# Kernel optimization log

Measured on AMD Instinct MI355X. Metric: run time of the kernel, lower is better.

The kernel has to match this reference:

```python
import jax, jax.numpy as jnp
import numpy as np

K = 20
EPS = 1e-5


def graph_feature(x, k=K):
    # x: [B, C, N] -> [B, 2C, N, k] (DGCNN edge features)
    xt = jnp.transpose(x, (0, 2, 1))                      # [B, N, C]
    sq = jnp.sum(xt * xt, axis=-1)                        # [B, N]
    inner = jnp.einsum('bnc,bmc->bnm', xt, xt)            # [B, N, N]
    neg_dist = 2.0 * inner - sq[:, :, None] - sq[:, None, :]
    idx = jax.lax.top_k(neg_dist, k)[1]                   # [B, N, k]
    nbr = jax.vmap(lambda f, i: f[i])(xt, idx)            # [B, N, k, C]
    ctr = jnp.broadcast_to(xt[:, :, None, :], nbr.shape)
    feat = jnp.concatenate([nbr - ctr, ctr], axis=-1)     # [B, N, k, 2C]
    return jnp.transpose(feat, (0, 3, 1, 2))              # [B, 2C, N, k]


def conv_bn_relu(x, W, g, b):
    # 1x1 conv (channel matmul) + BatchNorm (batch stats, training mode) + ReLU
    y = jnp.einsum('oc,bcnk->bonk', W, x)
    m = jnp.mean(y, axis=(0, 2, 3), keepdims=True)
    v = jnp.var(y, axis=(0, 2, 3), keepdims=True)
    yn = (y - m) * jax.lax.rsqrt(v + EPS)
    return jax.nn.relu(yn * g[None, :, None, None] + b[None, :, None, None])


def setup_inputs() -> dict:
    key = jax.random.key(0)
    ks = jax.random.split(key, 12)
    d = {'x': jax.random.normal(ks[0], (8, 3, 2048), dtype=jnp.float32)}
    chans = [(6, 64), (64, 64), (64, 128), (128, 256), (512, 512)]
    for i, (cin, cout) in enumerate(chans):
        d[f'W{i+1}'] = jax.random.normal(ks[i + 1], (cout, cin), dtype=jnp.float32) * (1.0 / np.sqrt(cin))
        d[f'g{i+1}'] = jnp.ones((cout,), dtype=jnp.float32)
        d[f'b{i+1}'] = jnp.zeros((cout,), dtype=jnp.float32)
    return d


def reference(x, W1, g1, b1, W2, g2, b2, W3, g3, b3, W4, g4, b4, W5, g5, b5):
    B, C, N = x.shape
    h = graph_feature(x)                                  # [B, 6, N, k]
    h = conv_bn_relu(h, W1, g1, b1)
    x1 = jnp.max(h, axis=-1, keepdims=True)               # [B, 64, N, 1]
    h = conv_bn_relu(h, W2, g2, b2)
    x2 = jnp.max(h, axis=-1, keepdims=True)
    h = conv_bn_relu(h, W3, g3, b3)
    x3 = jnp.max(h, axis=-1, keepdims=True)
    h = conv_bn_relu(h, W4, g4, b4)
    x4 = jnp.max(h, axis=-1, keepdims=True)
    cat = jnp.concatenate([x1, x2, x3, x4], axis=1)       # [B, 512, N, 1]
    out = conv_bn_relu(cat, W5, g5, b5)                   # [B, 512, N, 1]
    return out.reshape(B, -1, N)
```

## Files before the change

### kernel.cpp

```cpp
#include <hip/hip_runtime.h>
#include <hip/hip_bf16.h>

typedef _Float16 f16;
typedef _Float16 f16x8 __attribute__((ext_vector_type(8)));
typedef _Float16 f16x4 __attribute__((ext_vector_type(4)));
typedef float    f32x4 __attribute__((ext_vector_type(4)));
typedef unsigned long long u64;

constexpr int NB  = 8;
constexpr int NPT = 2048;
constexpr int KK  = 20;
constexpr int PT  = NB * NPT * KK;
constexpr int BNP = NB * NPT;
constexpr float EPS_BN = 1e-5f;
constexpr int NREP = 64;

constexpr size_t OFF_IDX = 0;
constexpr size_t OFF_WT1 = OFF_IDX + (size_t)BNP * KK * 4;
constexpr size_t OFF_WH2 = OFF_WT1 + 384 * 4;
constexpr size_t OFF_WH3 = OFF_WH2 + 4096 * 2;
constexpr size_t OFF_WH4 = OFF_WH3 + 8192 * 2;
constexpr size_t OFF_WH5 = OFF_WH4 + 32768 * 2;
constexpr size_t OFF_ST  = OFF_WH5 + 262144 * 2;
constexpr size_t OFF_SS  = OFF_ST + 5 * 1024 * 4;
constexpr size_t OFF_CAT = OFF_SS + 5 * 1024 * 4;
constexpr size_t OFF_Y3  = OFF_CAT + (size_t)BNP * 512 * 2;
constexpr size_t OFF_Y1  = OFF_Y3 + (size_t)PT * 64 * 2;
constexpr size_t OFF_Y2  = OFF_Y3 + (size_t)PT * 128 * 2;
constexpr size_t OFF_REP = OFF_Y2 + (size_t)PT * 64 * 2;
constexpr size_t WS_NEED = OFF_REP + (size_t)NREP * 1024 * 4;

__global__ void marker_kernel(float* __restrict__ out, float v) {
    if (threadIdx.x == 0 && blockIdx.x == 0) out[0] = v;
}

__device__ __forceinline__ void gload16(const f16* g, f16* ldsbase) {
    __builtin_amdgcn_global_load_lds(
        (const __attribute__((address_space(1))) void*)g,
        (__attribute__((address_space(3))) void*)ldsbase, 16, 0, 0);
}

__global__ __launch_bounds__(256) void prep_weights(
        const float* __restrict__ W1, const float* __restrict__ W2,
        const float* __restrict__ W3, const float* __restrict__ W4,
        const float* __restrict__ W5,
        float* __restrict__ wt1, f16* __restrict__ wh2, f16* __restrict__ wh3,
        f16* __restrict__ wh4, f16* __restrict__ wh5) {
    int i = blockIdx.x * 256 + threadIdx.x;
    if (i < 384)    { int o = i / 6, c = i - o * 6; wt1[c * 64 + o] = W1[i]; }
    if (i < 4096)   wh2[i] = (f16)W2[i];
    if (i < 8192)   wh3[i] = (f16)W3[i];
    if (i < 32768)  wh4[i] = (f16)W4[i];
    if (i < 262144) wh5[i] = (f16)W5[i];
}

__device__ __forceinline__ u64 mkkey(float d, int m) {
    unsigned u = __float_as_uint(d);
    u = (u & 0x80000000u) ? ~u : (u | 0x80000000u);
    return ((u64)u << 32) | (unsigned)(2047 - m);
}
__device__ __forceinline__ int key2m(u64 k) { return 2047 - (int)(k & 0xFFFFFFFFull); }

__device__ __forceinline__ void qins(u64 k, u64& q0, u64& q1, u64& q2, u64& q3, u64& spill) {
    bool c0 = k > q0, c1 = k > q1, c2 = k > q2, c3 = k > q3;
    u64 drop = c3 ? q3 : k;
    spill = spill > drop ? spill : drop;
    q3 = c2 ? q2 : (c3 ? k : q3);
    q2 = c1 ? q1 : (c2 ? k : q2);
    q1 = c0 ? q0 : (c1 ? k : q1);
    q0 = c0 ? k  : q0;
}

__global__ __launch_bounds__(256) void knn_kernel(const float* __restrict__ x,
                                                  int* __restrict__ idxo) {
    const int tid  = threadIdx.x;
    const int lane = tid & 63;
    const int wid  = tid >> 6;
    const int r    = blockIdx.x * 4 + wid;
    const int b    = r >> 11;
    const int n    = r & 2047;
    const float* xb = x + b * (3 * NPT);

    __shared__ float sqs[NPT];
    __shared__ int   cand[4][32];
#pragma unroll
    for (int i = 0; i < NPT / 256; ++i) {
        int m = i * 256 + tid;
        float a0 = xb[m], a1 = xb[NPT + m], a2 = xb[2 * NPT + m];
        sqs[m] = __fadd_rn(__fadd_rn(__fmul_rn(a0, a0), __fmul_rn(a1, a1)),
                           __fmul_rn(a2, a2));
    }
    __syncthreads();

    const float xn0 = xb[n], xn1 = xb[NPT + n], xn2 = xb[2 * NPT + n];
    const float sqn = sqs[n];

    auto dist2 = [&](int m) -> float {
        float dot = __fmaf_rn(xn0, xb[m],
                    __fmaf_rn(xn1, xb[NPT + m],
                    __fmul_rn(xn2, xb[2 * NPT + m])));
        return __fsub_rn(__fsub_rn(__fmul_rn(2.f, dot), sqn), sqs[m]);
    };

    u64 qa0 = 0, qa1 = 0, qa2 = 0, qa3 = 0, sA = 0;
    u64 qb0 = 0, qb1 = 0, qb2 = 0, qb3 = 0, sB = 0;
#pragma unroll
    for (int i = 0; i < 16; ++i) {
        int ma = i * 64 + lane;
        int mb = 1024 + ma;
        float da = dist2(ma);
        float db = dist2(mb);
        qins(mkkey(da, ma), qa0, qa1, qa2, qa3, sA);
        qins(mkkey(db, mb), qb0, qb1, qb2, qb3, sB);
    }
    u64 spill = sA > sB ? sA : sB;
    qins(qb0, qa0, qa1, qa2, qa3, spill);
    qins(qb1, qa0, qa1, qa2, qa3, spill);
    qins(qb2, qa0, qa1, qa2, qa3, spill);
    qins(qb3, qa0, qa1, qa2, qa3, spill);
    u64 q0 = qa0, q1 = qa1, q2 = qa2, q3 = qa3;

    int C;
    unsigned lo = 0u, hi = 0xFFFFFFFFu;
#pragma unroll 1
    for (int it = 0; it < 32 && lo < hi; ++it) {
        unsigned span = hi - lo;
        unsigned mid  = lo + (span >> 1) + (span & 1);
        u64 M = (u64)mid << 32;
        int cnt = __popcll(__ballot(q0 >= M)) + __popcll(__ballot(q1 >= M))
                + __popcll(__ballot(q2 >= M)) + __popcll(__ballot(q3 >= M));
        if (cnt >= 26) lo = mid; else hi = mid - 1;
    }
    const u64 T64 = (u64)lo << 32;

    u64 b0 = __ballot(q0 >= T64), b1 = __ballot(q1 >= T64);
    u64 b2 = __ballot(q2 >= T64), b3 = __ballot(q3 >= T64);
    int n0 = __popcll(b0), n1 = __popcll(b1), n2 = __popcll(b2), n3 = __popcll(b3);
    C = n0 + n1 + n2 + n3;
    bool conflict = (__ballot(spill >= T64) != 0ull) || (C > 32);

    if (!conflict) {
        u64 ltm = (1ull << lane) - 1ull;
        if (q0 >= T64) cand[wid][__popcll(b0 & ltm)] = key2m(q0);
        if (q1 >= T64) cand[wid][n0 + __popcll(b1 & ltm)] = key2m(q1);
        if (q2 >= T64) cand[wid][n0 + n1 + __popcll(b2 & ltm)] = key2m(q2);
        if (q3 >= T64) cand[wid][n0 + n1 + n2 + __popcll(b3 & ltm)] = key2m(q3);
    } else {
        C = 26;
#pragma unroll 1
        for (int t = 0; t < 26; ++t) {
            u64 v = q0;
#pragma unroll
            for (int s = 1; s < 64; s <<= 1) {
                u64 ov = __shfl_xor(v, s);
                if (ov > v) v = ov;
            }
            if (lane == 0) cand[wid][t] = key2m(v);
            if (q0 == v) {
                q0 = q1; q1 = q2; q2 = q3; q3 = 0;
                if (!(q0 > spill)) {
                    q0 = q1 = q2 = q3 = 0; spill = 0;
                    for (int ii = 0; ii < 32; ++ii) {
                        int mr = ii * 64 + lane;
                        u64 kr = mkkey(dist2(mr), mr);
                        if (kr < v) qins(kr, q0, q1, q2, q3, spill);
                    }
                }
            }
        }
    }
    __syncthreads();

    int mm = (lane < C) ? cand[wid][lane] : 0;
    const double dxn0 = (double)xn0, dxn1 = (double)xn1, dxn2 = (double)xn2;
    const double dsqn = dxn0 * dxn0 + dxn1 * dxn1 + dxn2 * dxn2;
    double xm0 = (double)xb[mm], xm1 = (double)xb[NPT + mm], xm2 = (double)xb[2 * NPT + mm];
    double ddot = dxn0 * xm0 + dxn1 * xm1 + dxn2 * xm2;
    double dsqm = xm0 * xm0 + xm1 * xm1 + xm2 * xm2;
    double dd   = 2.0 * ddot - dsqn - dsqm;

    int rank = 0;
#pragma unroll 1
    for (int s = 0; s < C; ++s) {
        double ds = __shfl(dd, s);
        int    ms = __shfl(mm, s);
        if (ds > dd || (ds == dd && ms < mm)) ++rank;
    }
    if (lane < C && rank < KK) idxo[rank * BNP + r] = mm;
}

__global__ __launch_bounds__(256) void conv1_kernel(const float* __restrict__ x,
                                                    const int* __restrict__ idx,
                                                    const float* __restrict__ Wt,
                                                    f16* __restrict__ y,
                                                    float* __restrict__ strep) {
    const int tid = threadIdx.x, lane = tid & 63, wid = tid >> 6;
    int p = blockIdx.x * 256 + tid;
    int r = p & (BNP - 1);
    int n = r & 2047;
    int b = r >> 11;
    int m = idx[p];
    const float* xb = x + b * (3 * NPT);
    float f3 = xb[n], f4 = xb[NPT + n], f5 = xb[2 * NPT + n];
    float f0 = xb[m] - f3, f1 = xb[NPT + m] - f4, f2 = xb[2 * NPT + m] - f5;
    float fv[6] = { f0, f1, f2, f3, f4, f5 };

    float acc[64];
#pragma unroll
    for (int o = 0; o < 64; ++o) acc[o] = 0.f;
#pragma unroll
    for (int c = 0; c < 6; ++c) {
        float hv = fv[c];
#pragma unroll
        for (int o = 0; o < 64; ++o) acc[o] = fmaf(Wt[c * 64 + o], hv, acc[o]);
    }
    f16* yp = y + (size_t)p * 64;
#pragma unroll
    for (int o = 0; o < 64; ++o) yp[o] = (f16)acc[o];

    __shared__ float lsum[4][64], lsq[4][64];
#pragma unroll
    for (int o = 0; o < 64; ++o) {
        float s = acc[o], q = acc[o] * acc[o];
#pragma unroll
        for (int off = 32; off >= 1; off >>= 1) { s += __shfl_xor(s, off); q += __shfl_xor(q, off); }
        if (lane == 0) { lsum[wid][o] = s; lsq[wid][o] = q; }
    }
    __syncthreads();
    float* rep = strep + ((blockIdx.x & (NREP - 1)) << 10);
    if (tid < 64) {
        atomicAdd(rep + tid,       lsum[0][tid] + lsum[1][tid] + lsum[2][tid] + lsum[3][tid]);
        atomicAdd(rep + 512 + tid, lsq[0][tid] + lsq[1][tid] + lsq[2][tid] + lsq[3][tid]);
    }
}

template<int CIN, int OBW>
__global__ __launch_bounds__(256) void conv_mfma_kernel(const f16* __restrict__ h,
                                                        const f16* __restrict__ W,
                                                        const f16* __restrict__ scshH,
                                                        f16* __restrict__ y,
                                                        float* __restrict__ strep) {
    constexpr int COUT = OBW * 64;
    const int tid = threadIdx.x, lane = tid & 63, wid = tid >> 6;
    const int lr = lane & 15, lg = lane >> 4;
    const int p0 = blockIdx.x * (256 / OBW) + (wid / OBW) * 64;
    const int ob = (wid & (OBW - 1)) * 64;

    f16x8 Bn[CIN / 32][4];
#pragma unroll
    for (int kt = 0; kt < CIN / 32; ++kt) {
        const int koff = kt * 32 + lg * 8;
        f16x8 scf = *(const f16x8*)(scshH + koff);
        f16x8 shf = *(const f16x8*)(scshH + 512 + koff);
#pragma unroll
        for (int pt = 0; pt < 4; ++pt) {
            f16x8 raw = *(const f16x8*)(h + (size_t)(p0 + pt * 16 + lr) * CIN + koff);
            f16x8 t = raw * scf + shf;
            f16x8 Bv;
#pragma unroll
            for (int e = 0; e < 8; ++e)
                Bv[e] = t[e] > (f16)0.f ? t[e] : (f16)0.f;
            Bn[kt][pt] = Bv;
        }
    }

    f32x4 acc[4][4];
#pragma unroll
    for (int pt = 0; pt < 4; ++pt)
#pragma unroll
        for (int t = 0; t < 4; ++t) acc[pt][t] = (f32x4){0.f, 0.f, 0.f, 0.f};

#pragma unroll
    for (int kt = 0; kt < CIN / 32; ++kt) {
        const int koff = kt * 32 + lg * 8;
        f16x8 A[4];
#pragma unroll
        for (int t = 0; t < 4; ++t)
            A[t] = *(const f16x8*)(W + (size_t)(ob + 16 * t + lr) * CIN + koff);
#pragma unroll
        for (int pt = 0; pt < 4; ++pt)
#pragma unroll
            for (int t = 0; t < 4; ++t)
                acc[pt][t] = __builtin_amdgcn_mfma_f32_16x16x32_f16(A[t], Bn[kt][pt], acc[pt][t], 0, 0, 0);
    }
#pragma unroll
    for (int pt = 0; pt < 4; ++pt) {
        int px = p0 + pt * 16 + lr;
#pragma unroll
        for (int t = 0; t < 4; ++t) {
            f16x4 v;
            v[0] = (f16)acc[pt][t][0]; v[1] = (f16)acc[pt][t][1];
            v[2] = (f16)acc[pt][t][2]; v[3] = (f16)acc[pt][t][3];
            *(f16x4*)(y + (size_t)px * COUT + ob + 16 * t + 4 * lg) = v;
        }
    }
    __shared__ float lsum[4][64], lsq[4][64];
#pragma unroll
    for (int t = 0; t < 4; ++t)
#pragma unroll
        for (int j = 0; j < 4; ++j) {
            float s = acc[0][t][j] + acc[1][t][j] + acc[2][t][j] + acc[3][t][j];
            float q = acc[0][t][j] * acc[0][t][j] + acc[1][t][j] * acc[1][t][j]
                    + acc[2][t][j] * acc[2][t][j] + acc[3][t][j] * acc[3][t][j];
#pragma unroll
            for (int m2 = 1; m2 < 16; m2 <<= 1) { s += __shfl_xor(s, m2); q += __shfl_xor(q, m2); }
            if (lr == 0) { lsum[wid][16 * t + 4 * lg + j] = s; lsq[wid][16 * t + 4 * lg + j] = q; }
        }
    __syncthreads();
    float* rep = strep + ((blockIdx.x & (NREP - 1)) << 10);
    if (tid < COUT) {
        int obIdx = tid >> 6, c = tid & 63;
        float S = 0.f, Q = 0.f;
#pragma unroll
        for (int w = obIdx; w < 4; w += OBW) { S += lsum[w][c]; Q += lsq[w][c]; }
        atomicAdd(rep + tid, S);
        atomicAdd(rep + 512 + tid, Q);
    }
}

__global__ __launch_bounds__(256) void conv4_fused_mfma(const f16* __restrict__ h,
                                                        const f16* __restrict__ W,
                                                        const f16* __restrict__ scshH,
                                                        float* __restrict__ strep,
                                                        f16* __restrict__ mx4,
                                                        f16* __restrict__ mn4,
                                                        f16* __restrict__ cat) {
    const int tid = threadIdx.x, lane = tid & 63, wid = tid >> 6;
    const int lr = lane & 15, lg = lane >> 4;
    const int r0 = blockIdx.x * 16;
    const int ob = wid * 64;

    __shared__ f16 sb[2][4][16][128];

    f32x4 rmax[4], rmin[4], rsum[4], rsq[4];
#pragma unroll
    for (int t = 0; t < 4; ++t) {
        rmax[t] = (f32x4){-3.3e38f, -3.3e38f, -3.3e38f, -3.3e38f};
        rmin[t] = (f32x4){ 3.3e38f,  3.3e38f,  3.3e38f,  3.3e38f};
        rsum[t] = (f32x4){0.f, 0.f, 0.f, 0.f};
        rsq[t]  = (f32x4){0.f, 0.f, 0.f, 0.f};
    }
    f16x8 im[4];
#pragma unroll
    for (int kt = 0; kt < 4; ++kt)
#pragma unroll
        for (int e = 0; e < 8; ++e) im[kt][e] = (f16)0.f;

    auto STAGE = [&](int buf, int kc) {
        const f16* gk = h + ((size_t)(kc * 4 + wid) * BNP + r0) * 128;
#pragma unroll
        for (int i = 0; i < 4; ++i) {
            int rr = i * 4 + (lane >> 4);
            int cc = (lane & 15) ^ rr;
            gload16(gk + (size_t)rr * 128 + cc * 8, &sb[buf][wid][i * 4][0]);
        }
    };

    STAGE(0, 0);
    __syncthreads();

    int cur = 0;
#pragma unroll 1
    for (int kc = 0; kc < 5; ++kc) {
        if (kc < 4) STAGE(cur ^ 1, kc + 1);

        f32x4 acc[4][4];
#pragma unroll
        for (int pt = 0; pt < 4; ++pt)
#pragma unroll
            for (int t = 0; t < 4; ++t) acc[pt][t] = (f32x4){0.f, 0.f, 0.f, 0.f};

#pragma unroll
        for (int kt = 0; kt < 4; ++kt) {
            const int koff = kt * 32 + lg * 8;
            f16x8 scf = *(const f16x8*)(scshH + koff);
            f16x8 shf = *(const f16x8*)(scshH + 512 + koff);
            f16x8 A[4];
#pragma unroll
            for (int t = 0; t < 4; ++t)
                A[t] = *(const f16x8*)(W + (size_t)(ob + 16 * t + lr) * 128 + koff);
            f16x8 Bv[4];
#pragma unroll
            for (int pt = 0; pt < 4; ++pt) {
                int cpos = (kt * 4 + lg) ^ lr;
                f16x8 raw = *(const f16x8*)(&sb[cur][pt][lr][cpos * 8]);
                f16x8 t = raw * scf + shf;
                f16x8 Bn;
#pragma unroll
                for (int e = 0; e < 8; ++e)
                    Bn[e] = t[e] > (f16)0.f ? t[e] : (f16)0.f;
                Bv[pt] = Bn;
            }
#pragma unroll
            for (int pt = 0; pt < 4; ++pt)
#pragma unroll
                for (int e = 0; e < 8; ++e)
                    im[kt][e] = (Bv[pt][e] > im[kt][e]) ? Bv[pt][e] : im[kt][e];
#pragma unroll
            for (int pt = 0; pt < 4; ++pt)
#pragma unroll
                for (int t = 0; t < 4; ++t)
                    acc[pt][t] = __builtin_amdgcn_mfma_f32_16x16x32_f16(A[t], Bv[pt], acc[pt][t], 0, 0, 0);
        }
#pragma unroll
        for (int pt = 0; pt < 4; ++pt)
#pragma unroll
            for (int t = 0; t < 4; ++t)
#pragma unroll
                for (int j = 0; j < 4; ++j) {
                    float v = acc[pt][t][j];
                    rmax[t][j] = fmaxf(rmax[t][j], v);
                    rmin[t][j] = fminf(rmin[t][j], v);
                    rsum[t][j] += v;
                    rsq[t][j]  += v * v;
                }
        __syncthreads();
        cur ^= 1;
    }

    if (wid == 0) {
#pragma unroll
        for (int kt = 0; kt < 4; ++kt)
            *(f16x8*)(cat + (size_t)(r0 + lr) * 512 + 128 + kt * 32 + lg * 8) = im[kt];
    }
#pragma unroll
    for (int t = 0; t < 4; ++t) {
        f16x4 vx, vn;
#pragma unroll
        for (int j = 0; j < 4; ++j) { vx[j] = (f16)rmax[t][j]; vn[j] = (f16)rmin[t][j]; }
        size_t base = (size_t)(r0 + lr) * 256 + ob + 16 * t + 4 * lg;
        *(f16x4*)(mx4 + base) = vx;
        *(f16x4*)(mn4 + base) = vn;
    }
    float* rep = strep + ((blockIdx.x & (NREP - 1)) << 10);
#pragma unroll
    for (int t = 0; t < 4; ++t)
#pragma unroll
        for (int j = 0; j < 4; ++j) {
            float s = rsum[t][j], q = rsq[t][j];
#pragma unroll
            for (int m2 = 1; m2 < 16; m2 <<= 1) { s += __shfl_xor(s, m2); q += __shfl_xor(q, m2); }
            if (lr == 0) {
                atomicAdd(rep + ob + 16 * t + 4 * lg + j, s);
                atomicAdd(rep + 512 + ob + 16 * t + 4 * lg + j, q);
            }
        }
}

__global__ __launch_bounds__(256) void cat4_kernel(const f16* __restrict__ mx4,
                                                   const f16* __restrict__ mn4,
                                                   const float* __restrict__ scsh,
                                                   f16* __restrict__ cat) {
    int i = blockIdx.x * 256 + threadIdx.x;
    int r = i >> 8, ch = i & 255;
    float sc = scsh[ch], sh = scsh[512 + ch];
    float v  = (sc > 0.f) ? (float)mx4[i] : (float)mn4[i];
    cat[(size_t)r * 512 + 256 + ch] = (f16)fmaxf(fmaf(v, sc, sh), 0.f);
}

__global__ __launch_bounds__(256) void conv5_mfma(const f16* __restrict__ cat,
                                                  const f16* __restrict__ W,
                                                  float* __restrict__ out,
                                                  float* __restrict__ strep) {
    const int tid = threadIdx.x;
    const int lane = tid & 63, wid = tid >> 6;
    const int lr = lane & 15, lg = lane >> 4;
    const int p0 = blockIdx.x * 64;
    const int ob = blockIdx.y * 256 + wid * 64;

    f32x4 acc[4][4];
#pragma unroll
    for (int pt = 0; pt < 4; ++pt)
#pragma unroll
        for (int t = 0; t < 4; ++t) acc[pt][t] = (f32x4){0.f, 0.f, 0.f, 0.f};

#pragma unroll
    for (int kt = 0; kt < 16; ++kt) {
        const int koff = kt * 32 + lg * 8;
        f16x8 A[4];
#pragma unroll
        for (int t = 0; t < 4; ++t)
            A[t] = *(const f16x8*)(W + (size_t)(ob + 16 * t + lr) * 512 + koff);
#pragma unroll
        for (int pt = 0; pt < 4; ++pt) {
            f16x8 B = *(const f16x8*)(cat + (size_t)(p0 + pt * 16 + lr) * 512 + koff);
#pragma unroll
            for (int t = 0; t < 4; ++t)
                acc[pt][t] = __builtin_amdgcn_mfma_f32_16x16x32_f16(A[t], B, acc[pt][t], 0, 0, 0);
        }
    }
#pragma unroll
    for (int pt = 0; pt < 4; ++pt) {
        int px = p0 + pt * 16 + lr;
        int b = px >> 11, n = px & 2047;
#pragma unroll
        for (int t = 0; t < 4; ++t) {
#pragma unroll
            for (int j = 0; j < 4; ++j) {
                int o = ob + 16 * t + 4 * lg + j;
                out[((size_t)(b * 512 + o)) * 2048 + n] = acc[pt][t][j];
            }
        }
    }
    __shared__ float lsum[4][64], lsq[4][64];
#pragma unroll
    for (int t = 0; t < 4; ++t)
#pragma unroll
        for (int j = 0; j < 4; ++j) {
            float s = acc[0][t][j] + acc[1][t][j] + acc[2][t][j] + acc[3][t][j];
            float q = acc[0][t][j] * acc[0][t][j] + acc[1][t][j] * acc[1][t][j]
                    + acc[2][t][j] * acc[2][t][j] + acc[3][t][j] * acc[3][t][j];
#pragma unroll
            for (int m2 = 1; m2 < 16; m2 <<= 1) { s += __shfl_xor(s, m2); q += __shfl_xor(q, m2); }
            if (lr == 0) { lsum[wid][16 * t + 4 * lg + j] = s; lsq[wid][16 * t + 4 * lg + j] = q; }
        }
    __syncthreads();
    float* rep = strep + ((blockIdx.x & (NREP - 1)) << 10);
    if (tid < 256) {
        int w = tid >> 6, c = tid & 63;
        atomicAdd(rep + blockIdx.y * 256 + tid, lsum[w][c]);
        atomicAdd(rep + 512 + blockIdx.y * 256 + tid, lsq[w][c]);
    }
}

__global__ void finalize_kernel(float* __restrict__ strep, const float* __restrict__ g,
                                const float* __restrict__ bb, float* __restrict__ scsh,
                                f16* __restrict__ scshH, int C, float invM) {
    int c = threadIdx.x;
    if (c < C) {
        float s = 0.f, q = 0.f;
#pragma unroll 4
        for (int rr = 0; rr < NREP; ++rr) {
            s += strep[rr * 1024 + c];
            q += strep[rr * 1024 + 512 + c];
        }
#pragma unroll 4
        for (int rr = 0; rr < NREP; ++rr) {
            strep[rr * 1024 + c] = 0.f;
            strep[rr * 1024 + 512 + c] = 0.f;
        }
        float mean = s * invM;
        float var  = q * invM - mean * mean;
        float istd = rsqrtf(var + EPS_BN);
        float sc   = g[c] * istd;
        float sh   = bb[c] - mean * sc;
        scsh[c]        = sc;
        scsh[512 + c]  = sh;
        scshH[c]       = (f16)sc;
        scshH[512 + c] = (f16)sh;
    }
}

template<int C>
__global__ __launch_bounds__(256) void catmax_vec(const f16* __restrict__ y,
                                                  const float* __restrict__ scsh,
                                                  f16* __restrict__ cat, int coff) {
    constexpr int CB = C / 8;
    int i  = blockIdx.x * 256 + threadIdx.x;
    int r  = i / CB;
    int cc = (i - r * CB) * 8;
    float sc[8], sh[8];
#pragma unroll
    for (int e = 0; e < 8; ++e) { sc[e] = scsh[cc + e]; sh[e] = scsh[512 + cc + e]; }
    float mx[8];
#pragma unroll
    for (int e = 0; e < 8; ++e) mx[e] = -3.3e38f;
#pragma unroll
    for (int k = 0; k < KK; ++k) {
        f16x8 v = *(const f16x8*)(y + ((size_t)k * BNP + r) * C + cc);
#pragma unroll
        for (int e = 0; e < 8; ++e)
            mx[e] = fmaxf(mx[e], fmaf((float)v[e], sc[e], sh[e]));
    }
    f16x8 o;
#pragma unroll
    for (int e = 0; e < 8; ++e) o[e] = (f16)fmaxf(mx[e], 0.f);
    *(f16x8*)(cat + (size_t)r * 512 + coff + cc) = o;
}

__global__ __launch_bounds__(256) void norm5_kernel(float* __restrict__ out,
                                                    const float* __restrict__ scsh) {
    int o = blockIdx.y;
    int r = blockIdx.x * 256 + threadIdx.x;
    int b = r >> 11, n = r & 2047;
    float sc = scsh[o], sh = scsh[512 + o];
    size_t i = ((size_t)(b * 512 + o)) * 2048 + n;
    float v = fmaf(out[i], sc, sh);
    out[i] = v > 0.f ? v : 0.f;
}

extern "C" void kernel_launch(void* const* d_in, const int* in_sizes, int n_in,
                              void* d_out, int out_size, void* d_ws, size_t ws_size,
                              hipStream_t stream) {
    float* out = (float*)d_out;
    if (ws_size < WS_NEED) {
        marker_kernel<<<1, 64, 0, stream>>>(out, 1000.0f + (float)(ws_size >> 20));
        return;
    }

    const float* x  = (const float*)d_in[0];
    const float* W1 = (const float*)d_in[1];
    const float* g1 = (const float*)d_in[2];
    const float* b1 = (const float*)d_in[3];
    const float* W2 = (const float*)d_in[4];
    const float* g2 = (const float*)d_in[5];
    const float* b2 = (const float*)d_in[6];
    const float* W3 = (const float*)d_in[7];
    const float* g3 = (const float*)d_in[8];
    const float* b3 = (const float*)d_in[9];
    const float* W4 = (const float*)d_in[10];
    const float* g4 = (const float*)d_in[11];
    const float* b4 = (const float*)d_in[12];
    const float* W5 = (const float*)d_in[13];
    const float* g5 = (const float*)d_in[14];
    const float* b5 = (const float*)d_in[15];

    char*  ws    = (char*)d_ws;
    int*   idx   = (int*)(ws + OFF_IDX);
    float* wt1   = (float*)(ws + OFF_WT1);
    f16*   wh2   = (f16*)(ws + OFF_WH2);
    f16*   wh3   = (f16*)(ws + OFF_WH3);
    f16*   wh4   = (f16*)(ws + OFF_WH4);
    f16*   wh5   = (f16*)(ws + OFF_WH5);
    f16*   scshH = (f16*)(ws + OFF_ST);
    float* scsh  = (float*)(ws + OFF_SS);
    f16*   cat   = (f16*)(ws + OFF_CAT);
    f16*   y1    = (f16*)(ws + OFF_Y1);
    f16*   y2    = (f16*)(ws + OFF_Y2);
    f16*   y3    = (f16*)(ws + OFF_Y3);
    f16*   mx4   = (f16*)(ws + OFF_Y2);
    f16*   mn4   = (f16*)(ws + OFF_Y2 + (size_t)BNP * 256 * 2);
    float* strep = (float*)(ws + OFF_REP);

    hipMemsetAsync(strep, 0, (size_t)NREP * 1024 * 4, stream);

    prep_weights<<<1024, 256, 0, stream>>>(W1, W2, W3, W4, W5, wt1, wh2, wh3, wh4, wh5);
    knn_kernel<<<4096, 256, 0, stream>>>(x, idx);

    const float invM  = 1.0f / (float)PT;
    const float invM5 = 1.0f / (float)BNP;

    conv1_kernel<<<PT / 256, 256, 0, stream>>>(x, idx, wt1, y1, strep);
    finalize_kernel<<<1, 512, 0, stream>>>(strep, g1, b1, scsh + 0, scshH + 0, 64, invM);
    catmax_vec<64><<<BNP * 8 / 256, 256, 0, stream>>>(y1, scsh + 0, cat, 0);

    conv_mfma_kernel<64, 1><<<PT / 256, 256, 0, stream>>>(y1, wh2, scshH + 0, y2, strep);
    finalize_kernel<<<1, 512, 0, stream>>>(strep, g2, b2, scsh + 1024, scshH + 1024, 64, invM);
    catmax_vec<64><<<BNP * 8 / 256, 256, 0, stream>>>(y2, scsh + 1024, cat, 64);

    conv_mfma_kernel<64, 2><<<PT / 128, 256, 0, stream>>>(y2, wh3, scshH + 1024, y3, strep);
    finalize_kernel<<<1, 512, 0, stream>>>(strep, g3, b3, scsh + 2048, scshH + 2048, 128, invM);

    conv4_fused_mfma<<<BNP / 16, 256, 0, stream>>>(y3, wh4, scshH + 2048, strep, mx4, mn4, cat);
    finalize_kernel<<<1, 512, 0, stream>>>(strep, g4, b4, scsh + 3072, scshH + 3072, 256, invM);
    cat4_kernel<<<BNP, 256, 0, stream>>>(mx4, mn4, scsh + 3072, cat);

    conv5_mfma<<<dim3(BNP / 64, 2), 256, 0, stream>>>(cat, wh5, out, strep);
    finalize_kernel<<<1, 512, 0, stream>>>(strep, g5, b5, scsh + 4096, scshH + 4096, 512, invM5);
    norm5_kernel<<<dim3(BNP / 256, 512), 256, 0, stream>>>(out, scsh + 4096);
}
```

Before: 401.8 us.

## Early-exit kNN threshold search, bitonic rank sort, and fp16 conv5 staging

The kNN kernel now stops its binary threshold search once the candidate count lands in the range 26 to 32, and falls back to the slow path if fewer than 26 remain. The serial shuffle-based rank loop is replaced by a wave-wide bitonic sort on packed keys (distance with index tiebreak). Conv5 writes pre-normalisation values as fp16 in a channel-major scratch buffer instead of fp32 into the output. norm5 then reads them vectorised and writes float4, which halves the intermediate traffic but adds fp16 rounding before BatchNorm.

```diff
diff --git a/kernel.cpp b/kernel.cpp
--- a/kernel.cpp
+++ b/kernel.cpp
@@ -120,7 +120,7 @@
     qins(qb3, qa0, qa1, qa2, qa3, spill);
     u64 q0 = qa0, q1 = qa1, q2 = qa2, q3 = qa3;
 
-    int C;
+    int C = 0;
     unsigned lo = 0u, hi = 0xFFFFFFFFu;
 #pragma unroll 1
     for (int it = 0; it < 32 && lo < hi; ++it) {
@@ -129,7 +129,10 @@
         u64 M = (u64)mid << 32;
         int cnt = __popcll(__ballot(q0 >= M)) + __popcll(__ballot(q1 >= M))
                 + __popcll(__ballot(q2 >= M)) + __popcll(__ballot(q3 >= M));
-        if (cnt >= 26) lo = mid; else hi = mid - 1;
+        if (cnt >= 26) {
+            lo = mid;
+            if (cnt <= 32) break;
+        } else hi = mid - 1;
     }
     const u64 T64 = (u64)lo << 32;
 
@@ -137,7 +140,7 @@
     u64 b2 = __ballot(q2 >= T64), b3 = __ballot(q3 >= T64);
     int n0 = __popcll(b0), n1 = __popcll(b1), n2 = __popcll(b2), n3 = __popcll(b3);
     C = n0 + n1 + n2 + n3;
-    bool conflict = (__ballot(spill >= T64) != 0ull) || (C > 32);
+    bool conflict = (__ballot(spill >= T64) != 0ull) || (C > 32) || (C < 26);
 
     if (!conflict) {
         u64 ltm = (1ull << lane) - 1ull;
@@ -179,14 +182,25 @@
     double dsqm = xm0 * xm0 + xm1 * xm1 + xm2 * xm2;
     double dd   = 2.0 * ddot - dsqn - dsqm;
 
-    int rank = 0;
-#pragma unroll 1
-    for (int s = 0; s < C; ++s) {
-        double ds = __shfl(dd, s);
-        int    ms = __shfl(mm, s);
-        if (ds > dd || (ds == dd && ms < mm)) ++rank;
-    }
-    if (lane < C && rank < KK) idxo[rank * BNP + r] = mm;
+    u64 ku = 0; unsigned tb = 0;
+    if (lane < C) {
+        u64 du = (u64)__double_as_longlong(dd);
+        ku = (du & 0x8000000000000000ull) ? ~du : (du | 0x8000000000000000ull);
+        tb = (unsigned)(2047 - mm);
+    }
+#pragma unroll
+    for (int k = 2; k <= 64; k <<= 1)
+#pragma unroll
+        for (int j = k >> 1; j > 0; j >>= 1) {
+            u64      ok = __shfl_xor(ku, j);
+            unsigned ot = __shfl_xor(tb, j);
+            bool dirDesc = ((lane & k) == 0);
+            bool lower   = ((lane & j) == 0);
+            bool myGT    = (ku > ok) || (ku == ok && tb > ot);
+            bool keep    = (myGT == (dirDesc == lower));
+            if (!keep) { ku = ok; tb = ot; }
+        }
+    if (lane < KK) idxo[lane * BNP + r] = 2047 - (int)tb;
 }
 
 __global__ __launch_bounds__(256) void conv1_kernel(const float* __restrict__ x,
@@ -460,7 +474,7 @@
 
 __global__ __launch_bounds__(256) void conv5_mfma(const f16* __restrict__ cat,
                                                   const f16* __restrict__ W,
-                                                  float* __restrict__ out,
+                                                  f16* __restrict__ y5,
                                                   float* __restrict__ strep) {
     const int tid = threadIdx.x;
     const int lane = tid & 63, wid = tid >> 6;
@@ -492,15 +506,13 @@
 #pragma unroll
     for (int pt = 0; pt < 4; ++pt) {
         int px = p0 + pt * 16 + lr;
-        int b = px >> 11, n = px & 2047;
-#pragma unroll
-        for (int t = 0; t < 4; ++t) {
+#pragma unroll
+        for (int t = 0; t < 4; ++t)
 #pragma unroll
             for (int j = 0; j < 4; ++j) {
                 int o = ob + 16 * t + 4 * lg + j;
-                out[((size_t)(b * 512 + o)) * 2048 + n] = acc[pt][t][j];
+                y5[(size_t)o * BNP + px] = (f16)acc[pt][t][j];
             }
-        }
     }
     __shared__ float lsum[4][64], lsq[4][64];
 #pragma unroll
@@ -578,15 +590,21 @@
     *(f16x8*)(cat + (size_t)r * 512 + coff + cc) = o;
 }
 
-__global__ __launch_bounds__(256) void norm5_kernel(float* __restrict__ out,
-                                                    const float* __restrict__ scsh) {
-    int o = blockIdx.y;
-    int r = blockIdx.x * 256 + threadIdx.x;
-    int b = r >> 11, n = r & 2047;
+__global__ __launch_bounds__(256) void norm5_kernel(const f16* __restrict__ y5,
+                                                    const float* __restrict__ scsh,
+                                                    float* __restrict__ out) {
+    int i  = blockIdx.x * 256 + threadIdx.x;
+    int o  = i >> 12;
+    int p4 = (i & 4095) * 4;
     float sc = scsh[o], sh = scsh[512 + o];
-    size_t i = ((size_t)(b * 512 + o)) * 2048 + n;
-    float v = fmaf(out[i], sc, sh);
-    out[i] = v > 0.f ? v : 0.f;
+    f16x4 v = *(const f16x4*)(y5 + (size_t)o * BNP + p4);
+    int b = p4 >> 11, n = p4 & 2047;
+    float4 w;
+    w.x = fmaxf(fmaf((float)v[0], sc, sh), 0.f);
+    w.y = fmaxf(fmaf((float)v[1], sc, sh), 0.f);
+    w.z = fmaxf(fmaf((float)v[2], sc, sh), 0.f);
+    w.w = fmaxf(fmaf((float)v[3], sc, sh), 0.f);
+    *(float4*)(out + ((size_t)(b * 512 + o)) * 2048 + n) = w;
 }
 
 extern "C" void kernel_launch(void* const* d_in, const int* in_sizes, int n_in,
@@ -630,6 +648,7 @@
     f16*   y3    = (f16*)(ws + OFF_Y3);
     f16*   mx4   = (f16*)(ws + OFF_Y2);
     f16*   mn4   = (f16*)(ws + OFF_Y2 + (size_t)BNP * 256 * 2);
+    f16*   y5    = (f16*)(ws + OFF_Y2);
     float* strep = (float*)(ws + OFF_REP);
 
     hipMemsetAsync(strep, 0, (size_t)NREP * 1024 * 4, stream);
@@ -655,7 +674,7 @@
     finalize_kernel<<<1, 512, 0, stream>>>(strep, g4, b4, scsh + 3072, scshH + 3072, 256, invM);
     cat4_kernel<<<BNP, 256, 0, stream>>>(mx4, mn4, scsh + 3072, cat);
 
-    conv5_mfma<<<dim3(BNP / 64, 2), 256, 0, stream>>>(cat, wh5, out, strep);
+    conv5_mfma<<<dim3(BNP / 64, 2), 256, 0, stream>>>(cat, wh5, y5, strep);
     finalize_kernel<<<1, 512, 0, stream>>>(strep, g5, b5, scsh + 4096, scshH + 4096, 512, invM5);
-    norm5_kernel<<<dim3(BNP / 256, 512), 256, 0, stream>>>(out, scsh + 4096);
-}
+    norm5_kernel<<<BNP * 512 / 4 / 256, 256, 0, stream>>>(y5, scsh + 4096, out);
+}
```

New measurement: 380.8 us. 1.06x faster.
